# Kernel tuning notes

Measured on AMD Instinct MI355X. Metric: run time of the kernel, lower is better.

Reference implementation:

```python
import jax, jax.numpy as jnp
import numpy as np

THETA = 100000.0

def _rope(x, pos, theta=THETA):
    # x: [..., H, S, d_k]; pos: [S] int
    d_k = x.shape[-1]
    half = d_k // 2
    inv_freq = theta ** (-(jnp.arange(half, dtype=jnp.float32) / half))  # theta^{-2i/d}
    ang = pos.astype(jnp.float32)[:, None] * inv_freq[None, :]  # [S, half]
    cos, sin = jnp.cos(ang), jnp.sin(ang)
    x1 = x[..., 0::2]
    x2 = x[..., 1::2]
    r1 = x1 * cos - x2 * sin
    r2 = x1 * sin + x2 * cos
    # interleave back to [..., d_k]
    return jnp.stack([r1, r2], axis=-1).reshape(x.shape)


def setup_inputs() -> dict:
    key = jax.random.key(0)
    ks = jax.random.split(key, 5)
    B, S, D = 1, 4096, 1024
    x = jax.random.normal(ks[0], (B, S, D), dtype=jnp.float32)
    sc = 1.0 / np.sqrt(D)
    Wq = jax.random.normal(ks[1], (D, D), dtype=jnp.float32) * sc
    Wk = jax.random.normal(ks[2], (D, D), dtype=jnp.float32) * sc
    Wv = jax.random.normal(ks[3], (D, D), dtype=jnp.float32) * sc
    Wo = jax.random.normal(ks[4], (D, D), dtype=jnp.float32) * sc
    token_positions = jnp.arange(S, dtype=jnp.int32)
    return {"x": x, "Wq": Wq, "Wk": Wk, "Wv": Wv, "Wo": Wo, "token_positions": token_positions}


def reference(x, Wq, Wk, Wv, Wo, token_positions):
    H = 16
    B, S, D = x.shape
    d_k = D // H
    # Linear (no bias): y = x @ W^T
    Q = jnp.einsum('bsd,ed->bse', x, Wq)
    K = jnp.einsum('bsd,ed->bse', x, Wk)
    V = jnp.einsum('bsd,ed->bse', x, Wv)
    # [B, H, S, d_k]
    Q = Q.reshape(B, S, H, d_k).transpose(0, 2, 1, 3)
    K = K.reshape(B, S, H, d_k).transpose(0, 2, 1, 3)
    V = V.reshape(B, S, H, d_k).transpose(0, 2, 1, 3)
    Q = _rope(Q, token_positions)
    K = _rope(K, token_positions)
    scores = jnp.einsum('bhqd,bhkd->bhqk', Q, K) / jnp.sqrt(jnp.float32(d_k))
    causal = jnp.tril(jnp.ones((S, S), dtype=bool))
    scores = jnp.where(causal, scores, jnp.finfo(scores.dtype).min)
    probs = jax.nn.softmax(scores, axis=-1)
    attn = jnp.einsum('bhqk,bhkd->bhqd', probs, V)
    attn = attn.transpose(0, 2, 1, 3).reshape(B, S, D)
    return jnp.einsum('bsd,ed->bse', attn, Wo)
```

## Files before the change

kernel.cpp:

```cpp
#include <hip/hip_runtime.h>

typedef float f32x4 __attribute__((ext_vector_type(4)));
typedef short s16x8 __attribute__((ext_vector_type(8)));
typedef int   i32x2 __attribute__((ext_vector_type(2)));
typedef int   i32x4 __attribute__((ext_vector_type(4)));

#define DEV static __device__ __forceinline__

DEV short f2bf(float f) {
    unsigned u = __builtin_bit_cast(unsigned, f);
    u += 0x7FFFu + ((u >> 16) & 1u);
    return (short)(u >> 16);
}
DEV float bf2f(short s) {
    return __builtin_bit_cast(float, ((unsigned)(unsigned short)s) << 16);
}
DEV int cvtpk(float lo, float hi) {
    int r;
    asm("v_cvt_pk_bf16_f32 %0, %1, %2" : "=v"(r) : "v"(lo), "v"(hi));
    return r;
}
DEV float fexp2(float x) { float r; asm("v_exp_f32 %0, %1" : "=v"(r) : "v"(x)); return r; }
DEV float ffract(float x){ float r; asm("v_fract_f32 %0, %1" : "=v"(r) : "v"(x)); return r; }
DEV float fsin(float x)  { float r; asm("v_sin_f32 %0, %1" : "=v"(r) : "v"(x)); return r; }
DEV float fcos(float x)  { float r; asm("v_cos_f32 %0, %1" : "=v"(r) : "v"(x)); return r; }
DEV f32x4 mfma_bf16(s16x8 a, s16x8 b, f32x4 c) {
    asm("v_mfma_f32_16x16x32_bf16 %0, %1, %2, %0" : "+v"(c) : "v"(a), "v"(b));
    return c;
}
DEV f32x4 mfma16_bf16(i32x2 a, i32x2 b, f32x4 c) {
    asm("v_mfma_f32_16x16x16_bf16 %0, %1, %2, %0" : "+v"(c) : "v"(a), "v"(b));
    return c;
}
DEV void gl_lds16(const void* g, void* l) {
    __builtin_amdgcn_global_load_lds((const __attribute__((address_space(1))) unsigned*)g,
                                     (__attribute__((address_space(3))) unsigned*)l, 16, 0, 0);
}

__global__ __launch_bounds__(256) void conv_kernel(
    const float* __restrict__ x,
    const float* __restrict__ W0, const float* __restrict__ W1,
    const float* __restrict__ W2, const float* __restrict__ W3,
    short* __restrict__ xb,
    short* __restrict__ B0, short* __restrict__ B1,
    short* __restrict__ B2, short* __restrict__ B3)
{
    const int bid = blockIdx.x, tid = threadIdx.x;
    const float* src;
    short* dst;
    size_t off;
    if (bid < 2048) {
        src = x; dst = xb; off = (size_t)bid * 2048 + tid * 8;
    } else {
        int t = bid - 2048, wi = t >> 9;
        src = wi == 0 ? W0 : (wi == 1 ? W1 : (wi == 2 ? W2 : W3));
        dst = wi == 0 ? B0 : (wi == 1 ? B1 : (wi == 2 ? B2 : B3));
        off = (size_t)(t & 511) * 2048 + tid * 8;
    }
    f32x4 v0 = *(const f32x4*)(src + off);
    f32x4 v1 = *(const f32x4*)(src + off + 4);
    s16x8 o;
    #pragma unroll
    for (int e = 0; e < 4; e++) { o[e] = f2bf(v0[e]); o[4 + e] = f2bf(v1[e]); }
    *(s16x8*)(dst + off) = o;
}

template<int BM, int OUT_BF16, int ROPE>
__global__ __launch_bounds__(256) void gemm128(
    const short* __restrict__ A,
    const short* __restrict__ Bq, const short* __restrict__ Bk, const short* __restrict__ Bv,
    void* __restrict__ Cq, void* __restrict__ Ck, void* __restrict__ Cv,
    const int* __restrict__ posp)
{
    constexpr int KD = 1024, ND = 1024;
    constexpr int MI = BM / 32;
    __shared__ __align__(16) short As[BM * 32];
    __shared__ __align__(16) short Bs[128 * 32];
    const int n0 = blockIdx.x * 128, m0 = blockIdx.y * BM;
    const int zz = blockIdx.z;
    const short* B = zz == 0 ? Bq : (zz == 1 ? Bk : Bv);
    void* C       = zz == 0 ? Cq : (zz == 1 ? Ck : Cv);
    const int tid = threadIdx.x;
    const int lane = tid & 63, w = tid >> 6, g = lane >> 4, c = lane & 15;
    const int wm = w >> 1, wn = w & 1;

    const int swz = (tid & 3) ^ ((tid >> 3) & 3);
    const short* a0 = A + (size_t)(m0 + (tid >> 2)) * KD + 8 * swz;
    const short* a1 = a0 + (size_t)64 * KD;
    const short* b0 = B + (size_t)(n0 + (tid >> 2)) * KD + 8 * swz;
    const short* b1 = b0 + (size_t)64 * KD;
    char* ldsA = (char*)As + w * 1024;
    char* ldsB = (char*)Bs + w * 1024;

    int aoff[MI], boff[4];
    #pragma unroll
    for (int i = 0; i < MI; i++) {
        int ar = wm * (BM / 2) + i * 16 + c;
        aoff[i] = ar * 64 + (g ^ ((ar >> 1) & 3)) * 16;
    }
    #pragma unroll
    for (int j = 0; j < 4; j++) {
        int br = wn * 64 + j * 16 + c;
        boff[j] = br * 64 + (g ^ ((br >> 1) & 3)) * 16;
    }

    f32x4 acc[MI][4] = {};

    for (int k0 = 0; k0 < KD; k0 += 32) {
        __syncthreads();
        gl_lds16(a0 + k0, ldsA);
        if (BM == 128) gl_lds16(a1 + k0, ldsA + 4096);
        gl_lds16(b0 + k0, ldsB);
        gl_lds16(b1 + k0, ldsB + 4096);
        __syncthreads();
        s16x8 af[MI], bf[4];
        #pragma unroll
        for (int i = 0; i < MI; i++) af[i] = *(const s16x8*)((const char*)As + aoff[i]);
        #pragma unroll
        for (int j = 0; j < 4; j++) bf[j] = *(const s16x8*)((const char*)Bs + boff[j]);
        #pragma unroll
        for (int i = 0; i < MI; i++)
            #pragma unroll
            for (int j = 0; j < 4; j++)
                acc[i][j] = mfma_bf16(af[i], bf[j], acc[i][j]);
    }

    if (ROPE && zz <= 1) {
        const float ps = (zz == 0) ? 0.18033688011112042f : 1.0f;
        #pragma unroll
        for (int j = 0; j < 4; j++) {
            int col = n0 + wn * 64 + j * 16 + c;
            float invf = fexp2(-(float)((col & 63) >> 1) * 0.51905126482615036f)
                       * 0.15915494309189535f;
            float ssign = (col & 1) ? 1.f : -1.f;
            #pragma unroll
            for (int i = 0; i < MI; i++)
                #pragma unroll
                for (int r = 0; r < 4; r++) {
                    int row = m0 + wm * (BM / 2) + i * 16 + 4 * g + r;
                    float fp = (float)posp[row];
                    float fr = ffract(fp * invf);
                    float sn = fsin(fr) * ps, cs = fcos(fr) * ps;
                    float own = acc[i][j][r];
                    float oth = __shfl_xor(own, 1);
                    acc[i][j][r] = own * cs + oth * (ssign * sn);
                }
        }
    }

    #pragma unroll
    for (int i = 0; i < MI; i++)
        #pragma unroll
        for (int j = 0; j < 4; j++)
            #pragma unroll
            for (int r = 0; r < 4; r++) {
                int row = m0 + wm * (BM / 2) + i * 16 + 4 * g + r;
                int col = n0 + wn * 64 + j * 16 + c;
                float v = acc[i][j][r];
                if (OUT_BF16) ((short*)C)[(size_t)row * ND + col] = f2bf(v);
                else          ((float*)C)[(size_t)row * ND + col] = v;
            }
}

template<int A_BF16, int OUT_BF16>
__global__ __launch_bounds__(256) void gemm_bt(
    const void* __restrict__ Ap,
    const float* __restrict__ B0, const float* __restrict__ B1, const float* __restrict__ B2,
    void* __restrict__ C0, void* __restrict__ C1, void* __restrict__ C2)
{
    constexpr int KD = 1024, ND = 1024;
    __shared__ short As[64][40];
    __shared__ short Bs[64][40];
    const int n0 = blockIdx.x * 64, m0 = blockIdx.y * 64;
    const float* Bw = blockIdx.z == 0 ? B0 : (blockIdx.z == 1 ? B1 : B2);
    void* Cw       = blockIdx.z == 0 ? C0 : (blockIdx.z == 1 ? C1 : C2);
    const int tid = threadIdx.x;
    const int lane = tid & 63, w = tid >> 6, g = lane >> 4, c = lane & 15;
    const int wm = w >> 1, wn = w & 1;
    const int sr = tid >> 2, scc = (tid & 3) * 8;

    f32x4 acc[2][2] = {};

    for (int k0 = 0; k0 < KD; k0 += 32) {
        __syncthreads();
        if (A_BF16) {
            *(s16x8*)&As[sr][scc] =
                *(const s16x8*)((const short*)Ap + (size_t)(m0 + sr) * KD + k0 + scc);
        } else {
            const float* ap = (const float*)Ap + (size_t)(m0 + sr) * KD + k0 + scc;
            f32x4 va = *(const f32x4*)ap, vb = *(const f32x4*)(ap + 4);
            s16x8 av;
            #pragma unroll
            for (int e = 0; e < 4; e++) { av[e] = f2bf(va[e]); av[4 + e] = f2bf(vb[e]); }
            *(s16x8*)&As[sr][scc] = av;
        }
        {
            const float* bp = Bw + (size_t)(n0 + sr) * KD + k0 + scc;
            f32x4 va = *(const f32x4*)bp, vb = *(const f32x4*)(bp + 4);
            s16x8 bv;
            #pragma unroll
            for (int e = 0; e < 4; e++) { bv[e] = f2bf(va[e]); bv[4 + e] = f2bf(vb[e]); }
            *(s16x8*)&Bs[sr][scc] = bv;
        }
        __syncthreads();
        s16x8 af[2], bfv[2];
        #pragma unroll
        for (int i = 0; i < 2; i++) af[i]  = *(const s16x8*)&As[wm * 32 + i * 16 + c][8 * g];
        #pragma unroll
        for (int j = 0; j < 2; j++) bfv[j] = *(const s16x8*)&Bs[wn * 32 + j * 16 + c][8 * g];
        #pragma unroll
        for (int i = 0; i < 2; i++)
            #pragma unroll
            for (int j = 0; j < 2; j++)
                acc[i][j] = mfma_bf16(af[i], bfv[j], acc[i][j]);
    }

    #pragma unroll
    for (int i = 0; i < 2; i++)
        #pragma unroll
        for (int j = 0; j < 2; j++)
            #pragma unroll
            for (int r = 0; r < 4; r++) {
                int row = m0 + wm * 32 + i * 16 + 4 * g + r;
                int col = n0 + wn * 32 + j * 16 + c;
                float v = acc[i][j][r];
                if (OUT_BF16) ((short*)Cw)[(size_t)row * ND + col] = f2bf(v);
                else          ((float*)Cw)[(size_t)row * ND + col] = v;
            }
}

__global__ __launch_bounds__(256) void rope_kernel(short* Q, short* K, const int* __restrict__ posp)
{
    const int t = blockIdx.x * 256 + threadIdx.x;
    const int isK = blockIdx.y;
    short* ptr = isK ? K : Q;
    const float postscale = isK ? 1.0f : 0.18033688011112042f;
    const int idx  = t * 8;
    const int srow = idx >> 10;
    const int dd   = (idx & 1023) & 63;
    const int p0   = dd >> 1;
    const float fp = (float)posp[srow];
    s16x8 v = *(s16x8*)(ptr + idx);
    s16x8 o;
    #pragma unroll
    for (int pr = 0; pr < 4; pr++) {
        float ex  = fexp2(-(float)(p0 + pr) * 0.51905126482615036f);
        float ang = fp * ex * 0.15915494309189535f;
        float fr  = ffract(ang);
        float sn  = fsin(fr) * postscale;
        float cs  = fcos(fr) * postscale;
        float x1 = bf2f(v[2 * pr]), x2 = bf2f(v[2 * pr + 1]);
        o[2 * pr]     = f2bf(x1 * cs - x2 * sn);
        o[2 * pr + 1] = f2bf(x1 * sn + x2 * cs);
    }
    *(s16x8*)(ptr + idx) = o;
}

template<int NZ>
__global__ __launch_bounds__(512, 2) void attn_kernel(
    const short* __restrict__ Q, const short* __restrict__ K,
    const short* __restrict__ V, short* __restrict__ O0,
    short* __restrict__ O1, short* __restrict__ O2, short* __restrict__ O3,
    float* __restrict__ Lf)
{
    constexpr int D = 1024;
    int qx, h, z;
    if (NZ > 1) {
        const int B = blockIdx.x;
        const int xcd = B & 7, k = B >> 3;
        h = xcd + 8 * (k / (16 * NZ));
        const int r = k % (16 * NZ);
        qx = r & 15;
        z = r >> 4;
    } else {
        qx = blockIdx.x; h = blockIdx.y; z = 0;
    }
    const int hc = h * 64;
    short* O = (z == 0) ? O0 : (z == 1 ? O1 : (z == 2 ? O2 : O3));
    const int tid = threadIdx.x;
    const int w = tid >> 6, lane = tid & 63, g = lane >> 4, c = lane & 15;

    __shared__ __align__(16) int Kl[2][64 * 32];
    __shared__ __align__(16) int Vl[2][64][32];

    const int wk = w & 3;
    const int krow_l = lane >> 3;
    const int kchunk = (lane & 7) ^ krow_l;
    const short* Kpre = K + hc + (size_t)(wk * 16 + krow_l) * D + kchunk * 8;
    char* kdst0 = (char*)&Kl[0][0] + wk * 16 * 128;
    char* kdst1 = (char*)&Kl[1][0] + wk * 16 * 128;

    const int vtid = tid & 255;
    const int vkvp = vtid & 31;
    const int vd0 = (vtid >> 5) * 8;
    const short* Vpre = V + hc + (size_t)(2 * vkvp) * D + vd0;

    int koff0[4], koff1[4];
    #pragma unroll
    for (int t = 0; t < 4; t++) {
        int row = t * 16 + c;
        koff0[t] = row * 128 + ((g) ^ (row & 7)) * 16;
        koff1[t] = row * 128 + ((4 + g) ^ (row & 7)) * 16;
    }

    for (int pi = 0; pi < 2; pi++) {
        const int qq = pi ? 31 - qx : qx;
        const int wq_min = qq * 128 + w * 16;
        const int qrow = wq_min + c;
        const short* qp = Q + (size_t)qrow * D + hc + 8 * g;
        const s16x8 bq0 = *(const s16x8*)qp;
        const s16x8 bq1 = *(const s16x8*)(qp + 32);

        f32x4 acc[4] = {};
        float l = 0.f;
        const int nkb = 2 * qq + 2;

        __syncthreads();
        s16x8 vs0, vs1;
        {
            if (w < 4) {
                gl_lds16(Kpre + (size_t)(z * 64) * D, kdst0);
                gl_lds16(Kpre + (size_t)(z * 64 + 8) * D, kdst0 + 8 * 128);
            } else {
                const short* vp = Vpre + (size_t)(z * 64) * D;
                vs0 = *(const s16x8*)vp;
                vs1 = *(const s16x8*)(vp + D);
            }
        }

        int cur = 0;
        for (int kb = z; kb < nkb; kb += NZ, cur ^= 1) {
            if (w >= 4) {
                #pragma unroll
                for (int e = 0; e < 8; e++) {
                    unsigned dw = (unsigned)(unsigned short)vs0[e] | ((unsigned)(unsigned short)vs1[e] << 16);
                    Vl[cur][vd0 + e][vkvp ^ (4 * e)] = (int)dw;
                }
            }
            asm volatile("s_waitcnt vmcnt(0)" ::: "memory");
            __syncthreads();

            const bool more = (kb + NZ) < nkb;
            if (more) {
                const int kb1 = kb + NZ;
                if (w < 4) {
                    char* kd = cur ? kdst0 : kdst1;
                    gl_lds16(Kpre + (size_t)(kb1 * 64) * D, kd);
                    gl_lds16(Kpre + (size_t)(kb1 * 64 + 8) * D, kd + 8 * 128);
                } else {
                    const short* vp = Vpre + (size_t)(kb1 * 64) * D;
                    vs0 = *(const s16x8*)vp;
                    vs1 = *(const s16x8*)(vp + D);
                }
            }

            if (kb * 64 > wq_min + 15) continue;

            const char* Kb = (const char*)&Kl[cur][0];
            f32x4 st[4];
            __builtin_amdgcn_s_setprio(1);
            #pragma unroll
            for (int t = 0; t < 4; t++) {
                s16x8 a0 = *(const s16x8*)(Kb + koff0[t]);
                s16x8 a1 = *(const s16x8*)(Kb + koff1[t]);
                f32x4 zf = {};
                zf = mfma_bf16(a0, bq0, zf);
                zf = mfma_bf16(a1, bq1, zf);
                st[t] = zf;
            }
            __builtin_amdgcn_s_setprio(0);

            float p[16];
            if (kb * 64 + 63 > wq_min) {
                #pragma unroll
                for (int t = 0; t < 4; t++)
                    #pragma unroll
                    for (int i = 0; i < 4; i++) {
                        int kv = kb * 64 + t * 16 + 4 * g + i;
                        float e = fexp2(st[t][i]);
                        if (kv > qrow) e = 0.f;
                        p[t * 4 + i] = e;
                        l += e;
                    }
            } else {
                #pragma unroll
                for (int t = 0; t < 4; t++)
                    #pragma unroll
                    for (int i = 0; i < 4; i++) {
                        float e = fexp2(st[t][i]);
                        p[t * 4 + i] = e;
                        l += e;
                    }
            }

            i32x2 pd[4];
            #pragma unroll
            for (int t = 0; t < 4; t++) {
                pd[t][0] = cvtpk(p[t * 4 + 0], p[t * 4 + 1]);
                pd[t][1] = cvtpk(p[t * 4 + 2], p[t * 4 + 3]);
            }

            __builtin_amdgcn_s_setprio(1);
            #pragma unroll
            for (int t = 0; t < 4; t++) {
                #pragma unroll
                for (int jt = 0; jt < 4; jt++) {
                    i32x2 vb = *(const i32x2*)&Vl[cur][jt * 16 + c][(t * 8 + 2 * g) ^ (4 * (c & 7))];
                    acc[jt] = mfma16_bf16(pd[t], vb, acc[jt]);
                }
            }
            __builtin_amdgcn_s_setprio(0);
        }

        float lsum = l + __shfl_xor(l, 16);
        lsum += __shfl_xor(lsum, 32);
        if (NZ > 1 && lane < 16) {
            float Lv = (lsum > 0.f) ? __log2f(lsum) : -1e30f;
            Lf[(size_t)(z * 16 + h) * 4096 + (qq * 128 + w * 16 + lane)] = Lv;
        }
        float linv[4];
        #pragma unroll
        for (int i = 0; i < 4; i++) {
            float ls = __shfl(lsum, 4 * g + i);
            linv[i] = (ls > 0.f) ? 1.f / ls : 0.f;
        }
        #pragma unroll
        for (int jt = 0; jt < 4; jt++)
            #pragma unroll
            for (int i = 0; i < 4; i++) {
                int r = qq * 128 + w * 16 + 4 * g + i;
                O[(size_t)r * D + hc + jt * 16 + c] = f2bf(acc[jt][i] * linv[i]);
            }
    }
}

template<int NP>
__global__ __launch_bounds__(256) void combine_kernel(
    short* __restrict__ Aw, const short* __restrict__ P1,
    const short* __restrict__ P2, const short* __restrict__ P3,
    const float* __restrict__ Lf)
{
    const int t = blockIdx.x * 256 + threadIdx.x;
    const int idx = t * 8;
    const int row = idx >> 10, col = idx & 1023, h = col >> 6;
    float L[NP];
    float LM = -1e30f;
    #pragma unroll
    for (int zi = 0; zi < NP; zi++) {
        L[zi] = Lf[(size_t)(zi * 16 + h) * 4096 + row];
        LM = fmaxf(LM, L[zi]);
    }
    float wz[NP], wsum = 0.f;
    #pragma unroll
    for (int zi = 0; zi < NP; zi++) { wz[zi] = fexp2(L[zi] - LM); wsum += wz[zi]; }
    float inv = 1.f / wsum;
    #pragma unroll
    for (int zi = 0; zi < NP; zi++) wz[zi] *= inv;

    const short* Ps[4] = {Aw, P1, P2, P3};
    f32x4 o0 = {}, o1 = {};
    #pragma unroll
    for (int zi = 0; zi < NP; zi++) {
        s16x8 a = *(const s16x8*)(Ps[zi] + idx);
        #pragma unroll
        for (int e = 0; e < 4; e++) o0[e] += wz[zi] * bf2f(a[e]);
        #pragma unroll
        for (int e = 0; e < 4; e++) o1[e] += wz[zi] * bf2f(a[4 + e]);
    }
    s16x8 o;
    #pragma unroll
    for (int e = 0; e < 4; e++) { o[e] = f2bf(o0[e]); o[4 + e] = f2bf(o1[e]); }
    *(s16x8*)(Aw + idx) = o;
}

extern "C" void kernel_launch(void* const* d_in, const int* in_sizes, int n_in,
                              void* d_out, int out_size, void* d_ws, size_t ws_size,
                              hipStream_t stream)
{
    const float* x  = (const float*)d_in[0];
    const float* Wq = (const float*)d_in[1];
    const float* Wk = (const float*)d_in[2];
    const float* Wv = (const float*)d_in[3];
    const float* Wo = (const float*)d_in[4];
    const int*  pos = (const int*)d_in[5];
    float* out = (float*)d_out;

    const size_t SD = (size_t)4096 * 1024;
    const size_t WSZ = (size_t)1024 * 1024;
    short* Qw = (short*)d_ws;
    short* Kw = Qw + SD;
    short* Vw = Kw + SD;
    short* Aw = Vw + SD;

    const size_t need_A4 = (7 * SD + 4 * WSZ) * sizeof(short) + 4 * 16 * 4096 * sizeof(float);
    const size_t need_A2 = (5 * SD + 4 * WSZ) * sizeof(short) + 2 * 16 * 4096 * sizeof(float);
    const size_t need_B  = (4 * SD + 4 * WSZ) * sizeof(short);

    if (ws_size >= need_A4) {
        short* P1  = Aw + SD;
        short* P2  = P1 + SD;
        short* P3  = P2 + SD;
        short* xb  = Aw;
        short* Wqb = P3 + SD;
        short* Wkb = Wqb + WSZ;
        short* Wvb = Wkb + WSZ;
        short* Wob = Wvb + WSZ;
        float* Lf  = (float*)(Wob + WSZ);
        conv_kernel<<<4096, 256, 0, stream>>>(x, Wq, Wk, Wv, Wo, xb, Wqb, Wkb, Wvb, Wob);
        gemm128<128, 1, 1><<<dim3(8, 32, 3), 256, 0, stream>>>(xb, Wqb, Wkb, Wvb, Qw, Kw, Vw, pos);
        attn_kernel<4><<<1024, 512, 0, stream>>>(Qw, Kw, Vw, Aw, P1, P2, P3, Lf);
        combine_kernel<4><<<2048, 256, 0, stream>>>(Aw, P1, P2, P3, Lf);
        gemm128<64, 0, 0><<<dim3(8, 64, 1), 256, 0, stream>>>(Aw, Wob, Wob, Wob, out, out, out, pos);
    } else if (ws_size >= need_A2) {
        short* P1  = Aw + SD;
        short* xb  = Aw;
        short* Wqb = P1 + SD;
        short* Wkb = Wqb + WSZ;
        short* Wvb = Wkb + WSZ;
        short* Wob = Wvb + WSZ;
        float* Lf  = (float*)(Wob + WSZ);
        conv_kernel<<<4096, 256, 0, stream>>>(x, Wq, Wk, Wv, Wo, xb, Wqb, Wkb, Wvb, Wob);
        gemm128<128, 1, 1><<<dim3(8, 32, 3), 256, 0, stream>>>(xb, Wqb, Wkb, Wvb, Qw, Kw, Vw, pos);
        attn_kernel<2><<<512, 512, 0, stream>>>(Qw, Kw, Vw, Aw, P1, P1, P1, Lf);
        combine_kernel<2><<<2048, 256, 0, stream>>>(Aw, P1, P1, P1, Lf);
        gemm128<64, 0, 0><<<dim3(8, 64, 1), 256, 0, stream>>>(Aw, Wob, Wob, Wob, out, out, out, pos);
    } else if (ws_size >= need_B) {
        short* xb  = Aw;
        short* Wqb = Aw + SD;
        short* Wkb = Wqb + WSZ;
        short* Wvb = Wkb + WSZ;
        short* Wob = Wvb + WSZ;
        conv_kernel<<<4096, 256, 0, stream>>>(x, Wq, Wk, Wv, Wo, xb, Wqb, Wkb, Wvb, Wob);
        gemm128<128, 1, 1><<<dim3(8, 32, 3), 256, 0, stream>>>(xb, Wqb, Wkb, Wvb, Qw, Kw, Vw, pos);
        attn_kernel<1><<<dim3(16, 16, 1), 512, 0, stream>>>(Qw, Kw, Vw, Aw, Aw, Aw, Aw, nullptr);
        gemm128<64, 0, 0><<<dim3(8, 64, 1), 256, 0, stream>>>(Aw, Wob, Wob, Wob, out, out, out, pos);
    } else {
        gemm_bt<0, 1><<<dim3(16, 64, 3), 256, 0, stream>>>(x, Wq, Wk, Wv, Qw, Kw, Vw);
        rope_kernel<<<dim3(2048, 2), 256, 0, stream>>>(Qw, Kw, pos);
        attn_kernel<1><<<dim3(16, 16, 1), 512, 0, stream>>>(Qw, Kw, Vw, Aw, Aw, Aw, Aw, nullptr);
        gemm_bt<1, 0><<<dim3(16, 64, 1), 256, 0, stream>>>(Aw, Wo, Wo, Wo, out, out, out);
    }
}
```

Baseline: 137.9 us.

## Give each attention wave two 16-row query tiles with 256-thread blocks

The attention kernel drops from 8 waves to 4 waves per block, and each wave now handles 32 query rows as two 16-row MFMA tiles that share the K and V fragments read from LDS. Every thread now helps load both K and V, so the old split of K-loading waves and V-loading waves is gone. The aim is to halve the LDS reads per unit of MFMA work and raise the compute-to-load ratio. In exchange it uses more registers per wave (two sets of accumulators and Q fragments), has fewer waves to hide latency, and masks causal tiles more coarsely at 32-row granularity.

```diff
diff --git a/kernel.cpp b/kernel.cpp
--- a/kernel.cpp
+++ b/kernel.cpp
@@ -257,7 +257,7 @@
 }
 
 template<int NZ>
-__global__ __launch_bounds__(512, 2) void attn_kernel(
+__global__ __launch_bounds__(256, 3) void attn_kernel(
     const short* __restrict__ Q, const short* __restrict__ K,
     const short* __restrict__ V, short* __restrict__ O0,
     short* __restrict__ O1, short* __restrict__ O2, short* __restrict__ O3,
@@ -283,16 +283,14 @@
     __shared__ __align__(16) int Kl[2][64 * 32];
     __shared__ __align__(16) int Vl[2][64][32];
 
-    const int wk = w & 3;
     const int krow_l = lane >> 3;
     const int kchunk = (lane & 7) ^ krow_l;
-    const short* Kpre = K + hc + (size_t)(wk * 16 + krow_l) * D + kchunk * 8;
-    char* kdst0 = (char*)&Kl[0][0] + wk * 16 * 128;
-    char* kdst1 = (char*)&Kl[1][0] + wk * 16 * 128;
-
-    const int vtid = tid & 255;
-    const int vkvp = vtid & 31;
-    const int vd0 = (vtid >> 5) * 8;
+    const short* Kpre = K + hc + (size_t)(w * 16 + krow_l) * D + kchunk * 8;
+    char* kdst0 = (char*)&Kl[0][0] + w * 16 * 128;
+    char* kdst1 = (char*)&Kl[1][0] + w * 16 * 128;
+
+    const int vkvp = tid & 31;
+    const int vd0 = (tid >> 5) * 8;
     const short* Vpre = V + hc + (size_t)(2 * vkvp) * D + vd0;
 
     int koff0[4], koff1[4];
@@ -305,37 +303,35 @@
 
     for (int pi = 0; pi < 2; pi++) {
         const int qq = pi ? 31 - qx : qx;
-        const int wq_min = qq * 128 + w * 16;
-        const int qrow = wq_min + c;
-        const short* qp = Q + (size_t)qrow * D + hc + 8 * g;
-        const s16x8 bq0 = *(const s16x8*)qp;
-        const s16x8 bq1 = *(const s16x8*)(qp + 32);
-
-        f32x4 acc[4] = {};
-        float l = 0.f;
+        const int wqb = qq * 128 + w * 32;
+        s16x8 bq[2][2];
+        #pragma unroll
+        for (int m = 0; m < 2; m++) {
+            const short* qp = Q + (size_t)(wqb + m * 16 + c) * D + hc + 8 * g;
+            bq[m][0] = *(const s16x8*)qp;
+            bq[m][1] = *(const s16x8*)(qp + 32);
+        }
+
+        f32x4 acc[2][4] = {};
+        float l2[2] = {0.f, 0.f};
         const int nkb = 2 * qq + 2;
 
         __syncthreads();
         s16x8 vs0, vs1;
         {
-            if (w < 4) {
-                gl_lds16(Kpre + (size_t)(z * 64) * D, kdst0);
-                gl_lds16(Kpre + (size_t)(z * 64 + 8) * D, kdst0 + 8 * 128);
-            } else {
-                const short* vp = Vpre + (size_t)(z * 64) * D;
-                vs0 = *(const s16x8*)vp;
-                vs1 = *(const s16x8*)(vp + D);
-            }
+            gl_lds16(Kpre + (size_t)(z * 64) * D, kdst0);
+            gl_lds16(Kpre + (size_t)(z * 64 + 8) * D, kdst0 + 8 * 128);
+            const short* vp = Vpre + (size_t)(z * 64) * D;
+            vs0 = *(const s16x8*)vp;
+            vs1 = *(const s16x8*)(vp + D);
         }
 
         int cur = 0;
         for (int kb = z; kb < nkb; kb += NZ, cur ^= 1) {
-            if (w >= 4) {
-                #pragma unroll
-                for (int e = 0; e < 8; e++) {
-                    unsigned dw = (unsigned)(unsigned short)vs0[e] | ((unsigned)(unsigned short)vs1[e] << 16);
-                    Vl[cur][vd0 + e][vkvp ^ (4 * e)] = (int)dw;
-                }
+            #pragma unroll
+            for (int e = 0; e < 8; e++) {
+                unsigned dw = (unsigned)(unsigned short)vs0[e] | ((unsigned)(unsigned short)vs1[e] << 16);
+                Vl[cur][vd0 + e][vkvp ^ (4 * e)] = (int)dw;
             }
             asm volatile("s_waitcnt vmcnt(0)" ::: "memory");
             __syncthreads();
@@ -343,61 +339,66 @@
             const bool more = (kb + NZ) < nkb;
             if (more) {
                 const int kb1 = kb + NZ;
-                if (w < 4) {
-                    char* kd = cur ? kdst0 : kdst1;
-                    gl_lds16(Kpre + (size_t)(kb1 * 64) * D, kd);
-                    gl_lds16(Kpre + (size_t)(kb1 * 64 + 8) * D, kd + 8 * 128);
-                } else {
-                    const short* vp = Vpre + (size_t)(kb1 * 64) * D;
-                    vs0 = *(const s16x8*)vp;
-                    vs1 = *(const s16x8*)(vp + D);
-                }
-            }
-
-            if (kb * 64 > wq_min + 15) continue;
+                char* kd = cur ? kdst0 : kdst1;
+                gl_lds16(Kpre + (size_t)(kb1 * 64) * D, kd);
+                gl_lds16(Kpre + (size_t)(kb1 * 64 + 8) * D, kd + 8 * 128);
+                const short* vp = Vpre + (size_t)(kb1 * 64) * D;
+                vs0 = *(const s16x8*)vp;
+                vs1 = *(const s16x8*)(vp + D);
+            }
+
+            if (kb * 64 > wqb + 31) continue;
 
             const char* Kb = (const char*)&Kl[cur][0];
-            f32x4 st[4];
+            f32x4 st[2][4];
             __builtin_amdgcn_s_setprio(1);
             #pragma unroll
             for (int t = 0; t < 4; t++) {
                 s16x8 a0 = *(const s16x8*)(Kb + koff0[t]);
                 s16x8 a1 = *(const s16x8*)(Kb + koff1[t]);
-                f32x4 zf = {};
-                zf = mfma_bf16(a0, bq0, zf);
-                zf = mfma_bf16(a1, bq1, zf);
-                st[t] = zf;
+                f32x4 z0 = {};
+                z0 = mfma_bf16(a0, bq[0][0], z0);
+                z0 = mfma_bf16(a1, bq[0][1], z0);
+                st[0][t] = z0;
+                f32x4 z1 = {};
+                z1 = mfma_bf16(a0, bq[1][0], z1);
+                z1 = mfma_bf16(a1, bq[1][1], z1);
+                st[1][t] = z1;
             }
             __builtin_amdgcn_s_setprio(0);
 
-            float p[16];
-            if (kb * 64 + 63 > wq_min) {
+            i32x2 pd[2][4];
+            #pragma unroll
+            for (int m = 0; m < 2; m++) {
+                const int wqm = wqb + m * 16;
+                const int qrow = wqm + c;
+                float p[16];
+                if (kb * 64 + 63 > wqm) {
+                    #pragma unroll
+                    for (int t = 0; t < 4; t++)
+                        #pragma unroll
+                        for (int i = 0; i < 4; i++) {
+                            int kv = kb * 64 + t * 16 + 4 * g + i;
+                            float e = fexp2(st[m][t][i]);
+                            if (kv > qrow) e = 0.f;
+                            p[t * 4 + i] = e;
+                            l2[m] += e;
+                        }
+                } else {
+                    #pragma unroll
+                    for (int t = 0; t < 4; t++)
+                        #pragma unroll
+                        for (int i = 0; i < 4; i++) {
+                            float e = fexp2(st[m][t][i]);
+                            p[t * 4 + i] = e;
+                            l2[m] += e;
+                        }
+                }
                 #pragma unroll
-                for (int t = 0; t < 4; t++)
-                    #pragma unroll
-                    for (int i = 0; i < 4; i++) {
-                        int kv = kb * 64 + t * 16 + 4 * g + i;
-                        float e = fexp2(st[t][i]);
-                        if (kv > qrow) e = 0.f;
-                        p[t * 4 + i] = e;
-                        l += e;
-                    }
-            } else {
-                #pragma unroll
-                for (int t = 0; t < 4; t++)
-                    #pragma unroll
-                    for (int i = 0; i < 4; i++) {
-                        float e = fexp2(st[t][i]);
-                        p[t * 4 + i] = e;
-                        l += e;
-                    }
-            }
-
-            i32x2 pd[4];
-            #pragma unroll
-            for (int t = 0; t < 4; t++) {
-                pd[t][0] = cvtpk(p[t * 4 + 0], p[t * 4 + 1]);
-                pd[t][1] = cvtpk(p[t * 4 + 2], p[t * 4 + 3]);
+                for (int t = 0; t < 4; t++) {
+                    pd[m][t][0] = cvtpk(p[t * 4 + 0], p[t * 4 + 1]);
+                    pd[m][t][1] = cvtpk(p[t * 4 + 2], p[t * 4 + 3]);
+                }
             }
 
             __builtin_amdgcn_s_setprio(1);
@@ -406,31 +407,35 @@
                 #pragma unroll
                 for (int jt = 0; jt < 4; jt++) {
                     i32x2 vb = *(const i32x2*)&Vl[cur][jt * 16 + c][(t * 8 + 2 * g) ^ (4 * (c & 7))];
-                    acc[jt] = mfma16_bf16(pd[t], vb, acc[jt]);
+                    acc[0][jt] = mfma16_bf16(pd[0][t], vb, acc[0][jt]);
+                    acc[1][jt] = mfma16_bf16(pd[1][t], vb, acc[1][jt]);
                 }
             }
             __builtin_amdgcn_s_setprio(0);
         }
 
-        float lsum = l + __shfl_xor(l, 16);
-        lsum += __shfl_xor(lsum, 32);
-        if (NZ > 1 && lane < 16) {
-            float Lv = (lsum > 0.f) ? __log2f(lsum) : -1e30f;
-            Lf[(size_t)(z * 16 + h) * 4096 + (qq * 128 + w * 16 + lane)] = Lv;
-        }
-        float linv[4];
-        #pragma unroll
-        for (int i = 0; i < 4; i++) {
-            float ls = __shfl(lsum, 4 * g + i);
-            linv[i] = (ls > 0.f) ? 1.f / ls : 0.f;
-        }
-        #pragma unroll
-        for (int jt = 0; jt < 4; jt++)
+        #pragma unroll
+        for (int m = 0; m < 2; m++) {
+            float lsum = l2[m] + __shfl_xor(l2[m], 16);
+            lsum += __shfl_xor(lsum, 32);
+            if (NZ > 1 && lane < 16) {
+                float Lv = (lsum > 0.f) ? __log2f(lsum) : -1e30f;
+                Lf[(size_t)(z * 16 + h) * 4096 + (wqb + m * 16 + lane)] = Lv;
+            }
+            float linv[4];
             #pragma unroll
             for (int i = 0; i < 4; i++) {
-                int r = qq * 128 + w * 16 + 4 * g + i;
-                O[(size_t)r * D + hc + jt * 16 + c] = f2bf(acc[jt][i] * linv[i]);
-            }
+                float ls = __shfl(lsum, 4 * g + i);
+                linv[i] = (ls > 0.f) ? 1.f / ls : 0.f;
+            }
+            #pragma unroll
+            for (int jt = 0; jt < 4; jt++)
+                #pragma unroll
+                for (int i = 0; i < 4; i++) {
+                    int r = wqb + m * 16 + 4 * g + i;
+                    O[(size_t)r * D + hc + jt * 16 + c] = f2bf(acc[m][jt][i] * linv[i]);
+                }
+        }
     }
 }
 
@@ -508,7 +513,7 @@
         float* Lf  = (float*)(Wob + WSZ);
         conv_kernel<<<4096, 256, 0, stream>>>(x, Wq, Wk, Wv, Wo, xb, Wqb, Wkb, Wvb, Wob);
         gemm128<128, 1, 1><<<dim3(8, 32, 3), 256, 0, stream>>>(xb, Wqb, Wkb, Wvb, Qw, Kw, Vw, pos);
-        attn_kernel<4><<<1024, 512, 0, stream>>>(Qw, Kw, Vw, Aw, P1, P2, P3, Lf);
+        attn_kernel<4><<<1024, 256, 0, stream>>>(Qw, Kw, Vw, Aw, P1, P2, P3, Lf);
         combine_kernel<4><<<2048, 256, 0, stream>>>(Aw, P1, P2, P3, Lf);
         gemm128<64, 0, 0><<<dim3(8, 64, 1), 256, 0, stream>>>(Aw, Wob, Wob, Wob, out, out, out, pos);
     } else if (ws_size >= need_A2) {
@@ -521,7 +526,7 @@
         float* Lf  = (float*)(Wob + WSZ);
         conv_kernel<<<4096, 256, 0, stream>>>(x, Wq, Wk, Wv, Wo, xb, Wqb, Wkb, Wvb, Wob);
         gemm128<128, 1, 1><<<dim3(8, 32, 3), 256, 0, stream>>>(xb, Wqb, Wkb, Wvb, Qw, Kw, Vw, pos);
-        attn_kernel<2><<<512, 512, 0, stream>>>(Qw, Kw, Vw, Aw, P1, P1, P1, Lf);
+        attn_kernel<2><<<512, 256, 0, stream>>>(Qw, Kw, Vw, Aw, P1, P1, P1, Lf);
         combine_kernel<2><<<2048, 256, 0, stream>>>(Aw, P1, P1, P1, Lf);
         gemm128<64, 0, 0><<<dim3(8, 64, 1), 256, 0, stream>>>(Aw, Wob, Wob, Wob, out, out, out, pos);
     } else if (ws_size >= need_B) {
@@ -532,12 +537,12 @@
         short* Wob = Wvb + WSZ;
         conv_kernel<<<4096, 256, 0, stream>>>(x, Wq, Wk, Wv, Wo, xb, Wqb, Wkb, Wvb, Wob);
         gemm128<128, 1, 1><<<dim3(8, 32, 3), 256, 0, stream>>>(xb, Wqb, Wkb, Wvb, Qw, Kw, Vw, pos);
-        attn_kernel<1><<<dim3(16, 16, 1), 512, 0, stream>>>(Qw, Kw, Vw, Aw, Aw, Aw, Aw, nullptr);
+        attn_kernel<1><<<dim3(16, 16, 1), 256, 0, stream>>>(Qw, Kw, Vw, Aw, Aw, Aw, Aw, nullptr);
         gemm128<64, 0, 0><<<dim3(8, 64, 1), 256, 0, stream>>>(Aw, Wob, Wob, Wob, out, out, out, pos);
     } else {
         gemm_bt<0, 1><<<dim3(16, 64, 3), 256, 0, stream>>>(x, Wq, Wk, Wv, Qw, Kw, Vw);
         rope_kernel<<<dim3(2048, 2), 256, 0, stream>>>(Qw, Kw, pos);
-        attn_kernel<1><<<dim3(16, 16, 1), 512, 0, stream>>>(Qw, Kw, Vw, Aw, Aw, Aw, Aw, nullptr);
+        attn_kernel<1><<<dim3(16, 16, 1), 256, 0, stream>>>(Qw, Kw, Vw, Aw, Aw, Aw, Aw, nullptr);
         gemm_bt<1, 0><<<dim3(16, 64, 1), 256, 0, stream>>>(Aw, Wo, Wo, Wo, out, out, out);
     }
 }
```

Result: faster. 134.3 us (-2.6%).
